# Optimization experiments

Measured on AMD Instinct MI355X. Metric: run time of the kernel, lower is better.

Reference implementation:

```python
import jax, jax.numpy as jnp
import numpy as np

HEAD_DIM = 64  # hidden_dim 1024 // heads_num 16


def setup_inputs() -> dict:
    key = jax.random.key(0)
    ks = jax.random.split(key, 5)
    B, S, H = 2, 4096, 1024
    std = 1.0 / np.sqrt(H)
    return {
        "x": jax.random.normal(ks[0], (B, S, H), jnp.float32),
        "Wq": jax.random.normal(ks[1], (H, H), jnp.float32) * std,
        "bq": jnp.zeros((H,), jnp.float32),
        "Wk": jax.random.normal(ks[2], (H, H), jnp.float32) * std,
        "bk": jnp.zeros((H,), jnp.float32),
        "Wv": jax.random.normal(ks[3], (H, H), jnp.float32) * std,
        "bv": jnp.zeros((H,), jnp.float32),
        "Wo": jax.random.normal(ks[4], (H, H), jnp.float32) * std,
        "bo": jnp.zeros((H,), jnp.float32),
    }


def reference(x, Wq, bq, Wk, bk, Wv, bv, Wo, bo):
    # Linear projections (torch Linear: x @ W^T + b)
    q = jnp.einsum("bsh,oh->bso", x, Wq) + bq
    k = jnp.einsum("bsh,oh->bso", x, Wk) + bk
    v = jnp.einsum("bsh,oh->bso", x, Wv) + bv
    # all_to_all is identity on a single device (world size 1)
    scale = jnp.float32(HEAD_DIM) ** 0.5
    # Faithful to source: attention over the FULL hidden dim (no head split),
    # full [B, S, S] score matrix.
    scores = jnp.einsum("bqh,bkh->bqk", q, k) / scale
    weights = jax.nn.softmax(scores, axis=-1)
    attn = jnp.einsum("bqk,bkh->bqh", weights, v)
    out = jnp.einsum("bsh,oh->bso", attn, Wo) + bo
    return out
```

## Files before the change

### kernel.cpp

```cpp
#include <hip/hip_runtime.h>
#include <stdint.h>


typedef __bf16 bf16x8 __attribute__((ext_vector_type(8)));
typedef float  f32x4  __attribute__((ext_vector_type(4)));

__device__ __forceinline__ unsigned short f32_to_bf16_rne(float f) {
    uint32_t u = __builtin_bit_cast(uint32_t, f);
    uint32_t r = (u + 0x7FFFu + ((u >> 16) & 1u)) >> 16;
    return (unsigned short)r;
}

#define BM 128
#define BN 128
#define BK 64

__global__ __launch_bounds__(256) void cvt_all(
    const float* __restrict__ x,
    const float* __restrict__ Wq, const float* __restrict__ Wk,
    const float* __restrict__ Wo, const float* __restrict__ Wv,
    const float* __restrict__ bv, const float* __restrict__ bo,
    unsigned short* __restrict__ x16, unsigned short* __restrict__ w16,
    float* __restrict__ rsum, float* __restrict__ bfinal)
{
    const int b = blockIdx.x, tid = threadIdx.x;
    if (b < 8192) {
        int i = (b * 256 + tid) * 4;
        float4 v = *(const float4*)(x + i);
        ushort4 o;
        o.x = f32_to_bf16_rne(v.x); o.y = f32_to_bf16_rne(v.y);
        o.z = f32_to_bf16_rne(v.z); o.w = f32_to_bf16_rne(v.w);
        *(ushort4*)(x16 + i) = o;
    } else if (b < 11264) {
        int bb = b - 8192;
        int which = bb >> 10;
        const float* src = which == 0 ? Wq : which == 1 ? Wk : Wo;
        int i = ((bb & 1023) * 256 + tid) * 4;
        float4 v = *(const float4*)(src + i);
        ushort4 o;
        o.x = f32_to_bf16_rne(v.x); o.y = f32_to_bf16_rne(v.y);
        o.z = f32_to_bf16_rne(v.z); o.w = f32_to_bf16_rne(v.w);
        *(ushort4*)(w16 + (size_t)which * 1048576 + i) = o;
    } else if (b < 11520) {
        __shared__ unsigned short tl[64 * 68];
        int t = b - 11264, tr = t >> 4, tc = t & 15;
        #pragma unroll
        for (int it = 0; it < 4; ++it) {
            int r  = it * 16 + (tid >> 4);
            int c0 = (tid & 15) * 4;
            float4 v = *(const float4*)(Wv + (size_t)(tr * 64 + r) * 1024 + tc * 64 + c0);
            tl[(c0 + 0) * 68 + r] = f32_to_bf16_rne(v.x);
            tl[(c0 + 1) * 68 + r] = f32_to_bf16_rne(v.y);
            tl[(c0 + 2) * 68 + r] = f32_to_bf16_rne(v.z);
            tl[(c0 + 3) * 68 + r] = f32_to_bf16_rne(v.w);
        }
        __syncthreads();
        #pragma unroll
        for (int it = 0; it < 4; ++it) {
            int c  = it * 16 + (tid >> 4);
            int r0 = (tid & 15) * 4;
            ushort4 o;
            o.x = tl[c * 68 + r0 + 0]; o.y = tl[c * 68 + r0 + 1];
            o.z = tl[c * 68 + r0 + 2]; o.w = tl[c * 68 + r0 + 3];
            *(ushort4*)(w16 + (size_t)3 * 1048576 + (size_t)(tc * 64 + c) * 1024 + tr * 64 + r0) = o;
        }
    } else if (b < 11536) {
        int bb = b - 11520;
        int lane = tid & 63, wv_ = tid >> 6;
        int rowBase = bb * 64 + wv_ * 16;
        for (int rr = 0; rr < 16; ++rr) {
            int row = rowBase + rr;
            float partial = 0.f;
            #pragma unroll
            for (int t2 = 0; t2 < 16; ++t2) {
                int h = t2 * 64 + lane;
                partial += Wo[(size_t)row * 1024 + h] * bv[h];
            }
            #pragma unroll
            for (int off = 32; off > 0; off >>= 1)
                partial += __shfl_xor(partial, off, 64);
            if (lane == 0) bfinal[row] = bo[row] + partial;
        }
    } else {
        int i = ((b - 11536) * 256 + tid) * 4;
        *(float4*)(rsum + i) = float4{0.f, 0.f, 0.f, 0.f};
    }
}

__device__ __forceinline__ void gemm_core(
    const unsigned short* __restrict__ Ab,
    const unsigned short* __restrict__ Bb,
    unsigned short* ldsA, unsigned short* ldsB,
    int mBase, int nBase, int lane, int wave, int K, f32x4 (&acc)[4][4])
{
    const int quad = lane >> 4;
    const int l16  = lane & 15;
    const int wr   = wave >> 1;
    const int wc   = wave & 1;

    for (int k0 = 0; k0 < K; k0 += BK) {
        #pragma unroll
        for (int i = 0; i < 4; ++i) {
            int base = (i * 4 + wave) * 64;
            int s    = base + lane;
            int row  = s >> 3;
            int col  = ((s ^ (s >> 3)) & 7) * 8;
            __builtin_amdgcn_global_load_lds(
                (const __attribute__((address_space(1))) void*)(Ab + (size_t)(mBase + row) * K + (size_t)(k0 + col)),
                (__attribute__((address_space(3))) void*)(&ldsA[base * 8]),
                16, 0, 0);
        }
        #pragma unroll
        for (int i = 0; i < 4; ++i) {
            int base = (i * 4 + wave) * 64;
            int s    = base + lane;
            int row  = s >> 3;
            int col  = ((s ^ (s >> 3)) & 7) * 8;
            __builtin_amdgcn_global_load_lds(
                (const __attribute__((address_space(1))) void*)(Bb + (size_t)(nBase + row) * K + (size_t)(k0 + col)),
                (__attribute__((address_space(3))) void*)(&ldsB[base * 8]),
                16, 0, 0);
        }
        __syncthreads();

        #pragma unroll
        for (int kk = 0; kk < 2; ++kk) {
            bf16x8 af[4], bfv[4];
            #pragma unroll
            for (int mi = 0; mi < 4; ++mi) {
                int r = wr * 64 + mi * 16 + l16;
                int c = kk * 4 + quad;
                af[mi] = *(const bf16x8*)(&ldsA[r * BK + (((c ^ r) & 7) << 3)]);
            }
            #pragma unroll
            for (int ni = 0; ni < 4; ++ni) {
                int r = wc * 64 + ni * 16 + l16;
                int c = kk * 4 + quad;
                bfv[ni] = *(const bf16x8*)(&ldsB[r * BK + (((c ^ r) & 7) << 3)]);
            }
            #pragma unroll
            for (int mi = 0; mi < 4; ++mi)
                #pragma unroll
                for (int ni = 0; ni < 4; ++ni)
                    acc[mi][ni] = __builtin_amdgcn_mfma_f32_16x16x32_bf16(
                        af[mi], bfv[ni], acc[mi][ni], 0, 0, 0);
        }
        __syncthreads();
    }
}

template <int MODE>
__global__ __launch_bounds__(256) void gemm_bt(
    const unsigned short* __restrict__ A,
    const unsigned short* __restrict__ Bt,
    void* __restrict__ C,
    const float* __restrict__ b0, float* __restrict__ rowsum,
    float alpha, int M, int N, int K,
    long long aZ, long long bZ, long long cZ)
{
    __shared__ unsigned short ldsA[BM * BK];
    __shared__ unsigned short ldsB[BN * BK];

    const int NB = gridDim.x, MBt = gridDim.y;
    int l  = blockIdx.x + gridDim.x * (blockIdx.y + gridDim.y * blockIdx.z);
    int xcd = l & 7;
    int t   = l >> 3;
    int MBX = MBt >> 1;
    int NBX = NB >> 2;
    int mbl = t % MBX;
    int r1  = t / MBX;
    int nbi = r1 % NBX;
    int zb  = r1 / NBX;
    int mb  = (xcd >> 2) * MBX + mbl;
    int nb  = (xcd & 3) * NBX + nbi;

    const unsigned short* Ab = A  + (size_t)zb * aZ;
    const unsigned short* Bb = Bt + (size_t)zb * bZ;

    const int tid  = threadIdx.x;
    const int lane = tid & 63;
    const int wave = tid >> 6;
    const int quad = lane >> 4;
    const int l16  = lane & 15;
    const int wr   = wave >> 1;
    const int wc   = wave & 1;
    const int mBase = mb * BM;
    const int nBase = nb * BN;

    f32x4 acc[4][4] = {};
    gemm_core(Ab, Bb, ldsA, ldsB, mBase, nBase, lane, wave, K, acc);

    if (MODE == 1) {
        unsigned short* Cz = (unsigned short*)C + (size_t)zb * cZ;
        #pragma unroll
        for (int mi = 0; mi < 4; ++mi)
            #pragma unroll
            for (int ni = 0; ni < 4; ++ni) {
                int col = nBase + wc * 64 + ni * 16 + l16;
                float b = b0 ? b0[col] : 0.f;
                #pragma unroll
                for (int r = 0; r < 4; ++r) {
                    int row = mBase + wr * 64 + mi * 16 + quad * 4 + r;
                    Cz[(size_t)row * N + col] = f32_to_bf16_rne(acc[mi][ni][r] + b);
                }
            }
    } else if (MODE == 3) {
        unsigned short* Pz = (unsigned short*)C + (size_t)zb * cZ;
        float* rs = rowsum + (size_t)zb * M;
        #pragma unroll
        for (int mi = 0; mi < 4; ++mi) {
            #pragma unroll
            for (int r = 0; r < 4; ++r) {
                int row = mBase + wr * 64 + mi * 16 + quad * 4 + r;
                float e[4];
                float partial = 0.f;
                #pragma unroll
                for (int ni = 0; ni < 4; ++ni) {
                    e[ni] = __expf(acc[mi][ni][r] * alpha);
                    partial += e[ni];
                }
                #pragma unroll
                for (int ni = 0; ni < 4; ++ni) {
                    int col = nBase + wc * 64 + ni * 16 + l16;
                    Pz[(size_t)row * N + col] = f32_to_bf16_rne(e[ni]);
                }
                #pragma unroll
                for (int off = 1; off < 16; off <<= 1)
                    partial += __shfl_xor(partial, off, 64);
                if (l16 == 0) atomicAdd(&rs[row], partial);
            }
        }
    } else {
        float* Cz = (float*)C + (size_t)zb * cZ;
        const float* rs = rowsum + (size_t)zb * M;
        #pragma unroll
        for (int mi = 0; mi < 4; ++mi) {
            #pragma unroll
            for (int r = 0; r < 4; ++r) {
                int row = mBase + wr * 64 + mi * 16 + quad * 4 + r;
                float inv = 1.f / rs[row];
                #pragma unroll
                for (int ni = 0; ni < 4; ++ni) {
                    int col = nBase + wc * 64 + ni * 16 + l16;
                    Cz[(size_t)row * N + col] = acc[mi][ni][r] * inv + b0[col];
                }
            }
        }
    }
}

__global__ __launch_bounds__(256) void gemm_qkf(
    const unsigned short* __restrict__ x16,
    const unsigned short* __restrict__ w16,
    unsigned short* __restrict__ q16,
    unsigned short* __restrict__ k16,
    unsigned short* __restrict__ F16,
    const float* __restrict__ bq, const float* __restrict__ bk)
{
    __shared__ unsigned short ldsA[BM * BK];
    __shared__ unsigned short ldsB[BN * BK];

    int l   = blockIdx.x;
    int idx = (l & 7) * 136 + (l >> 3);

    const unsigned short *Ab, *Bb;
    unsigned short* Cb;
    const float* bias;
    int mBase, nBase;
    if (idx < 1024) {
        int role = idx >> 9;
        int s    = idx & 511;
        mBase = (s >> 3) * BM; nBase = (s & 7) * BN;
        Ab = x16; Bb = w16 + (size_t)role * 1048576;
        Cb = role ? k16 : q16; bias = role ? bk : bq;
    } else {
        int f = idx - 1024;
        mBase = (f >> 3) * BM; nBase = (f & 7) * BN;
        Ab = w16 + (size_t)2 * 1048576;
        Bb = w16 + (size_t)3 * 1048576;
        Cb = F16; bias = nullptr;
    }

    const int tid  = threadIdx.x;
    const int lane = tid & 63;
    const int wave = tid >> 6;
    const int quad = lane >> 4;
    const int l16  = lane & 15;
    const int wr   = wave >> 1;
    const int wc   = wave & 1;

    f32x4 acc[4][4] = {};
    gemm_core(Ab, Bb, ldsA, ldsB, mBase, nBase, lane, wave, 1024, acc);

    #pragma unroll
    for (int mi = 0; mi < 4; ++mi)
        #pragma unroll
        for (int ni = 0; ni < 4; ++ni) {
            int col = nBase + wc * 64 + ni * 16 + l16;
            float b = bias ? bias[col] : 0.f;
            #pragma unroll
            for (int r = 0; r < 4; ++r) {
                int row = mBase + wr * 64 + mi * 16 + quad * 4 + r;
                Cb[(size_t)row * 1024 + col] = f32_to_bf16_rne(acc[mi][ni][r] + b);
            }
        }
}

extern "C" void kernel_launch(void* const* d_in, const int* in_sizes, int n_in,
                              void* d_out, int out_size, void* d_ws, size_t ws_size,
                              hipStream_t stream)
{
    const float* x  = (const float*)d_in[0];
    const float* Wq = (const float*)d_in[1];
    const float* bq = (const float*)d_in[2];
    const float* Wk = (const float*)d_in[3];
    const float* bk = (const float*)d_in[4];
    const float* Wv = (const float*)d_in[5];
    const float* bv = (const float*)d_in[6];
    const float* Wo = (const float*)d_in[7];
    const float* bo = (const float*)d_in[8];
    float* out = (float*)d_out;

    const int S = 4096, H = 1024, Bsz = 2;
    const int M = Bsz * S;

    char* p = (char*)d_ws;
    auto alloc = [&](size_t bytes) -> char* {
        char* r = p; p += (bytes + 255) & ~(size_t)255; return r;
    };
    unsigned short* w16  = (unsigned short*)alloc((size_t)4 * H * H * 2);
    unsigned short* F16  = (unsigned short*)alloc((size_t)H * H * 2);
    unsigned short* q16  = (unsigned short*)alloc((size_t)M * H * 2);
    unsigned short* k16  = (unsigned short*)alloc((size_t)M * H * 2);
    unsigned short* vot16= (unsigned short*)alloc((size_t)Bsz * H * S * 2);
    float*          rsum = (float*)alloc((size_t)M * 4);
    float*          bfin = (float*)alloc((size_t)H * 4);
    char* region = alloc((size_t)Bsz * S * S * 2);
    unsigned short* x16 = (unsigned short*)region;
    unsigned short* p16 = (unsigned short*)region;

    cvt_all<<<11544, 256, 0, stream>>>(x, Wq, Wk, Wo, Wv, bv, bo,
                                       x16, w16, rsum, bfin);

    gemm_qkf<<<1088, 256, 0, stream>>>(x16, w16, q16, k16, F16, bq, bk);

    gemm_bt<1><<<dim3(S / BN, H / BM, 2), 256, 0, stream>>>(
        F16, x16, vot16, nullptr, nullptr, 1.f, H, S, 1024,
        0, (long long)S * H, (long long)H * S);

    gemm_bt<3><<<dim3(S / BN, S / BM, 2), 256, 0, stream>>>(
        q16, k16, p16, nullptr, rsum, 0.125f, S, S, 1024,
        (long long)S * H, (long long)S * H, (long long)S * S);

    gemm_bt<6><<<dim3(H / BN, S / BM, 2), 256, 0, stream>>>(
        p16, vot16, out, bfin, rsum, 1.f, S, H, 4096,
        (long long)S * S, (long long)H * S, (long long)S * H);
}
```

Before: 365.9 us.

## Add pipelined 8-wave GEMM with direct-to-LDS loads for attention GEMMs

Introduces a new 512-thread GEMM kernel with larger tiles (256x256 for QK^T, 128x256 for PV). It uses global_load_lds with XOR-swizzled LDS, double buffering, phased prefetch interleaved with MFMA, setprio, and XCD-aware block remapping. The two largest GEMMs (scores with exp/rowsum epilogue, and the PV product with normalization) move to it, while the old modes are removed from gemm_bt. This aims to raise MFMA utilization and hide global load latency, at the cost of more LDS and register pressure and a rigid schedule that assumes K is a multiple of 64.

After: 371.6 us. Within noise of the previous version (+1.6%).

```diff
diff --git a/kernel.cpp b/kernel.cpp
--- a/kernel.cpp
+++ b/kernel.cpp
@@ -204,48 +204,6 @@
                     Cz[(size_t)row * N + col] = f32_to_bf16_rne(acc[mi][ni][r] + b);
                 }
             }
-    } else if (MODE == 3) {
-        unsigned short* Pz = (unsigned short*)C + (size_t)zb * cZ;
-        float* rs = rowsum + (size_t)zb * M;
-        #pragma unroll
-        for (int mi = 0; mi < 4; ++mi) {
-            #pragma unroll
-            for (int r = 0; r < 4; ++r) {
-                int row = mBase + wr * 64 + mi * 16 + quad * 4 + r;
-                float e[4];
-                float partial = 0.f;
-                #pragma unroll
-                for (int ni = 0; ni < 4; ++ni) {
-                    e[ni] = __expf(acc[mi][ni][r] * alpha);
-                    partial += e[ni];
-                }
-                #pragma unroll
-                for (int ni = 0; ni < 4; ++ni) {
-                    int col = nBase + wc * 64 + ni * 16 + l16;
-                    Pz[(size_t)row * N + col] = f32_to_bf16_rne(e[ni]);
-                }
-                #pragma unroll
-                for (int off = 1; off < 16; off <<= 1)
-                    partial += __shfl_xor(partial, off, 64);
-                if (l16 == 0) atomicAdd(&rs[row], partial);
-            }
-        }
-    } else {
-        float* Cz = (float*)C + (size_t)zb * cZ;
-        const float* rs = rowsum + (size_t)zb * M;
-        #pragma unroll
-        for (int mi = 0; mi < 4; ++mi) {
-            #pragma unroll
-            for (int r = 0; r < 4; ++r) {
-                int row = mBase + wr * 64 + mi * 16 + quad * 4 + r;
-                float inv = 1.f / rs[row];
-                #pragma unroll
-                for (int ni = 0; ni < 4; ++ni) {
-                    int col = nBase + wc * 64 + ni * 16 + l16;
-                    Cz[(size_t)row * N + col] = acc[mi][ni][r] * inv + b0[col];
-                }
-            }
-        }
     }
 }
 
@@ -306,6 +264,201 @@
         }
 }
 
+template <int MODE, int BMt, int BNt>
+__global__ __launch_bounds__(512) void gemm8p(
+    const unsigned short* __restrict__ A,
+    const unsigned short* __restrict__ Bt,
+    void* __restrict__ C,
+    const float* __restrict__ b0, float* __restrict__ rowsum,
+    float alpha, int M, int N, int K,
+    long long aZ, long long bZ, long long cZ,
+    int MBt, int NB)
+{
+    constexpr int RW  = BMt / 2;
+    constexpr int CW  = BNt / 4;
+    constexpr int MI  = RW / 16;
+    constexpr int NI  = CW / 16;
+    constexpr int NPH = MI / 2;
+    constexpr int BL  = (BNt * 64 / 512) / 8;
+    constexpr int NWT = BL + NPH - 1;
+
+    __shared__ __align__(16) unsigned short ldsA[2][BMt * 64];
+    __shared__ __align__(16) unsigned short ldsB[2][BNt * 64];
+
+    const int l   = blockIdx.x;
+    const int xcd = l & 7;
+    const int t   = l >> 3;
+    const int MBX = MBt >> 1;
+    const int NBX = NB >> 2;
+    const int mbl = t % MBX;
+    const int r1  = t / MBX;
+    const int nbi = r1 % NBX;
+    const int zb  = r1 / NBX;
+    const int mb  = (xcd >> 2) * MBX + mbl;
+    const int nb  = (xcd & 3) * NBX + nbi;
+
+    const unsigned short* Ab = A  + (size_t)zb * aZ;
+    const unsigned short* Bb = Bt + (size_t)zb * bZ;
+
+    const int tid  = threadIdx.x;
+    const int lane = tid & 63;
+    const int wave = tid >> 6;
+    const int quad = lane >> 4;
+    const int l16  = lane & 15;
+    const int wr   = wave >> 2;
+    const int wc   = wave & 3;
+    const int mBase = mb * BMt;
+    const int nBase = nb * BNt;
+    const int NT    = K >> 6;
+
+    const int aRow0 = ((wave & 4) ? RW : 0) + (wave & 3) * 8;
+
+    auto stageA = [&](int p, int kt, int q) {
+        const int rowbase = aRow0 + q * 32;
+        const int row = rowbase + (lane >> 3);
+        const int col = (((lane & 7) ^ row) & 7) << 3;
+        __builtin_amdgcn_global_load_lds(
+            (const __attribute__((address_space(1))) void*)(
+                Ab + (size_t)(mBase + row) * K + (size_t)((kt << 6) + col)),
+            (__attribute__((address_space(3))) void*)(&ldsA[p][rowbase * 64]),
+            16, 0, 0);
+    };
+    auto stageB = [&](int p, int kt) {
+        #pragma unroll
+        for (int i = 0; i < BL; ++i) {
+            const int g   = wave * BL + i;
+            const int row = (g << 3) + (lane >> 3);
+            const int col = (((lane & 7) ^ row) & 7) << 3;
+            __builtin_amdgcn_global_load_lds(
+                (const __attribute__((address_space(1))) void*)(
+                    Bb + (size_t)(nBase + row) * K + (size_t)((kt << 6) + col)),
+                (__attribute__((address_space(3))) void*)(&ldsB[p][g << 9]),
+                16, 0, 0);
+        }
+    };
+
+    bf16x8 bf[NI][2];
+    bf16x8 af[2][2];
+    auto ldB = [&](int p) {
+        #pragma unroll
+        for (int n2 = 0; n2 < NI; ++n2)
+            #pragma unroll
+            for (int kk = 0; kk < 2; ++kk) {
+                const int r = wc * CW + n2 * 16 + l16;
+                const int c = kk * 4 + quad;
+                bf[n2][kk] = *(const bf16x8*)&ldsB[p][r * 64 + (((c ^ r) & 7) << 3)];
+            }
+    };
+    auto ldA = [&](int p, int q) {
+        #pragma unroll
+        for (int m2 = 0; m2 < 2; ++m2)
+            #pragma unroll
+            for (int kk = 0; kk < 2; ++kk) {
+                const int r = wr * RW + (q * 2 + m2) * 16 + l16;
+                const int c = kk * 4 + quad;
+                af[m2][kk] = *(const bf16x8*)&ldsA[p][r * 64 + (((c ^ r) & 7) << 3)];
+            }
+    };
+
+    f32x4 acc[MI][NI] = {};
+
+    stageB(0, 0);
+    #pragma unroll
+    for (int q = 0; q < NPH; ++q) stageA(0, 0, q);
+    if (NT > 1) {
+        stageB(1, 1);
+        #pragma unroll
+        for (int q = 0; q < NPH - 1; ++q) stageA(1, 1, q);
+        asm volatile("s_waitcnt vmcnt(%0)" :: "n"(NWT) : "memory");
+    } else {
+        asm volatile("s_waitcnt vmcnt(0)" ::: "memory");
+    }
+    __builtin_amdgcn_s_barrier();
+
+    for (int kt = 0; kt < NT; ++kt) {
+        const int p = kt & 1;
+        #pragma unroll
+        for (int q = 0; q < NPH; ++q) {
+            if (q == 0) ldB(p);
+            ldA(p, q);
+            if (q == 0) {
+                if (kt + 1 < NT) stageA(p ^ 1, kt + 1, NPH - 1);
+            } else if (q == 1) {
+                if (kt + 2 < NT) { stageB(p, kt + 2); stageA(p, kt + 2, 0); }
+            } else {
+                if (kt + 2 < NT) stageA(p, kt + 2, q - 1);
+            }
+            if (q == NPH - 1) {
+                if (kt + 2 < NT) {
+                    asm volatile("s_waitcnt vmcnt(%0)" :: "n"(NWT) : "memory");
+                } else if (kt + 1 < NT) {
+                    asm volatile("s_waitcnt vmcnt(0)" ::: "memory");
+                }
+            }
+            __builtin_amdgcn_sched_barrier(0);
+            __builtin_amdgcn_s_barrier();
+            __builtin_amdgcn_sched_barrier(0);
+            __builtin_amdgcn_s_setprio(1);
+            #pragma unroll
+            for (int m2 = 0; m2 < 2; ++m2)
+                #pragma unroll
+                for (int n2 = 0; n2 < NI; ++n2)
+                    #pragma unroll
+                    for (int kk = 0; kk < 2; ++kk)
+                        acc[q * 2 + m2][n2] = __builtin_amdgcn_mfma_f32_16x16x32_bf16(
+                            af[m2][kk], bf[n2][kk], acc[q * 2 + m2][n2], 0, 0, 0);
+            __builtin_amdgcn_s_setprio(0);
+            __builtin_amdgcn_sched_barrier(0);
+            __builtin_amdgcn_s_barrier();
+            __builtin_amdgcn_sched_barrier(0);
+        }
+    }
+
+    if constexpr (MODE == 3) {
+        unsigned short* Pz = (unsigned short*)C + (size_t)zb * cZ;
+        float* rs = rowsum + (size_t)zb * M;
+        #pragma unroll
+        for (int mi = 0; mi < MI; ++mi) {
+            #pragma unroll
+            for (int r = 0; r < 4; ++r) {
+                const int row = mBase + wr * RW + mi * 16 + quad * 4 + r;
+                float e[NI];
+                float partial = 0.f;
+                #pragma unroll
+                for (int ni = 0; ni < NI; ++ni) {
+                    e[ni] = __expf(acc[mi][ni][r] * alpha);
+                    partial += e[ni];
+                }
+                #pragma unroll
+                for (int ni = 0; ni < NI; ++ni) {
+                    const int col = nBase + wc * CW + ni * 16 + l16;
+                    Pz[(size_t)row * N + col] = f32_to_bf16_rne(e[ni]);
+                }
+                #pragma unroll
+                for (int off = 1; off < 16; off <<= 1)
+                    partial += __shfl_xor(partial, off, 64);
+                if (l16 == 0) atomicAdd(&rs[row], partial);
+            }
+        }
+    } else {
+        float* Cz = (float*)C + (size_t)zb * cZ;
+        const float* rs = rowsum + (size_t)zb * M;
+        #pragma unroll
+        for (int mi = 0; mi < MI; ++mi) {
+            #pragma unroll
+            for (int r = 0; r < 4; ++r) {
+                const int row = mBase + wr * RW + mi * 16 + quad * 4 + r;
+                const float inv = 1.f / rs[row];
+                #pragma unroll
+                for (int ni = 0; ni < NI; ++ni) {
+                    const int col = nBase + wc * CW + ni * 16 + l16;
+                    Cz[(size_t)row * N + col] = acc[mi][ni][r] * inv + b0[col];
+                }
+            }
+        }
+    }
+}
+
 extern "C" void kernel_launch(void* const* d_in, const int* in_sizes, int n_in,
                               void* d_out, int out_size, void* d_ws, size_t ws_size,
                               hipStream_t stream)
@@ -348,11 +501,11 @@
         F16, x16, vot16, nullptr, nullptr, 1.f, H, S, 1024,
         0, (long long)S * H, (long long)H * S);
 
-    gemm_bt<3><<<dim3(S / BN, S / BM, 2), 256, 0, stream>>>(
+    gemm8p<3, 256, 256><<<512, 512, 0, stream>>>(
         q16, k16, p16, nullptr, rsum, 0.125f, S, S, 1024,
-        (long long)S * H, (long long)S * H, (long long)S * S);
-
-    gemm_bt<6><<<dim3(H / BN, S / BM, 2), 256, 0, stream>>>(
+        (long long)S * H, (long long)S * H, (long long)S * S, 16, 16);
+
+    gemm8p<6, 128, 256><<<256, 512, 0, stream>>>(
         p16, vot16, out, bfin, rsum, 1.f, S, H, 4096,
-        (long long)S * S, (long long)H * S, (long long)S * H);
-}
+        (long long)S * S, (long long)H * S, (long long)S * H, 32, 4);
+}
```
